# Kernel tuning notes

Hardware: AMD Instinct MI355X
Metric: run time of the kernel (lower is better)

The kernel has to match this reference:

```python
import jax, jax.numpy as jnp
import numpy as np

B = 64            # graphs per batch
NODES_PER_GRAPH = 1008  # 12 snapshots * 84 nodes
N = B * NODES_PER_GRAPH # 64512 total nodes
E = N * 16              # ~1M edges
SNAP = 12
SEG = 84
D_IN = 84
D_H = 128
EPS_BN = 1e-5


def setup_inputs() -> dict:
    key = jax.random.key(0)
    ks = jax.random.split(key, 20)
    s = 0.05  # small init scale for numerical sanity
    return {
        "x": jax.random.normal(ks[0], (N, D_IN), jnp.float32),
        "edge_index": jax.random.randint(ks[1], (2, E), 0, N, jnp.int64),
        "w1": jax.random.normal(ks[2], (D_IN, D_H), jnp.float32) * s,
        "b1": jax.random.normal(ks[3], (D_H,), jnp.float32) * s,
        "w2": jax.random.normal(ks[4], (D_H, D_H), jnp.float32) * s,
        "b2": jax.random.normal(ks[5], (D_H,), jnp.float32) * s,
        "pe": jax.random.normal(ks[6], (NODES_PER_GRAPH, D_H), jnp.float32) * s,
        "wf1": jax.random.normal(ks[7], (SNAP * 4 * D_H, 512), jnp.float32) * s,
        "bf1": jax.random.normal(ks[8], (512,), jnp.float32) * s,
        "g1": jnp.ones((512,), jnp.float32),
        "be1": jnp.zeros((512,), jnp.float32),
        "wf2": jax.random.normal(ks[9], (512, 32), jnp.float32) * s,
        "bf2": jax.random.normal(ks[10], (32,), jnp.float32) * s,
        "g2": jnp.ones((32,), jnp.float32),
        "be2": jnp.zeros((32,), jnp.float32),
        "wf3": jax.random.normal(ks[11], (32, 2), jnp.float32) * s,
        "bf3": jax.random.normal(ks[12], (2,), jnp.float32) * s,
    }


def _batch_norm(h, g, b):
    # training-mode BN: biased batch statistics, eps=1e-5 (torch default)
    mu = jnp.mean(h, axis=0)
    var = jnp.var(h, axis=0)
    return (h - mu) * jax.lax.rsqrt(var + EPS_BN) * g + b


def reference(x, edge_index, w1, b1, w2, b2, pe, wf1, bf1, g1, be1,
              wf2, bf2, g2, be2, wf3, bf3):
    src, dst = edge_index[0], edge_index[1]
    n = x.shape[0]
    b = n // NODES_PER_GRAPH

    # GINConv (eps=0, sum aggregation): h = Linear(x + sum_{j->i} x_j)
    agg1 = jax.ops.segment_sum(x[src], dst, num_segments=n)
    h1 = (x + agg1) @ w1 + b1                      # [N,128]
    agg2 = jax.ops.segment_sum(h1[src], dst, num_segments=n)
    h2 = (h1 + agg2) @ w2 + b2                     # [N,128]

    # positional encoding + full self-attention per graph (1008 tokens)
    h2 = h2.reshape(b, NODES_PER_GRAPH, D_H) + pe  # [B,1008,128]
    score = jnp.einsum('bqd,bkd->bqk', h2, h2) / np.sqrt(float(D_H))
    attn = jax.nn.softmax(score, axis=-1)
    ctx = jnp.einsum('bqk,bkd->bqd', attn, h2)     # [B,1008,128]

    # segmented max/mean pooling: blocks of 84 nodes, 12 snapshots per graph
    h1s = h1.reshape(b, SNAP, SEG, D_H)
    h2s = ctx.reshape(b, SNAP, SEG, D_H)
    feat = jnp.concatenate([
        jnp.max(h1s, axis=2), jnp.mean(h1s, axis=2),
        jnp.max(h2s, axis=2), jnp.mean(h2s, axis=2),
    ], axis=-1)                                    # [B,12,512]
    feat = feat.reshape(b, SNAP * 4 * D_H)         # [B,6144]

    # MLP head (dropout = identity at eval; BN in training-stat mode)
    out = _batch_norm(jax.nn.silu(feat @ wf1 + bf1), g1, be1)
    out = _batch_norm(jax.nn.silu(out @ wf2 + bf2), g2, be2)
    out = jax.nn.softmax(out @ wf3 + bf3, axis=1)  # [B,2]
    return out
```

## Files before the change

kernel.cpp:

```cpp
#include <hip/hip_runtime.h>
#include <math.h>

#define N_NODES 64512
#define DIN 84
#define XHP 96
#define KP 96
#define USP 104
#define DH 128
#define NPG 1008
#define BG 64
#define NSNAP 12
#define NSEG 84
#define NEDGE (N_NODES * 16)
#define DEGCAP 64
#define NBUCK 252
#define EPB 4096
#define BCAP 4608
#define ATT_SCALE 0.08838834764831845f

typedef __bf16 bf16_t;
typedef __bf16 bf16x8 __attribute__((ext_vector_type(8)));
typedef __bf16 bf16x4 __attribute__((ext_vector_type(4)));
typedef float f32x4 __attribute__((ext_vector_type(4)));
typedef _Float16 f16_t;
typedef _Float16 f16x4 __attribute__((ext_vector_type(4)));
typedef _Float16 f16x8 __attribute__((ext_vector_type(8)));

__device__ __forceinline__ f32x4 up4(f16x4 v) {
    return (f32x4){(float)v[0], (float)v[1], (float)v[2], (float)v[3]};
}

__global__ __launch_bounds__(256) void cvt_xh(const float* __restrict__ x,
                                              f16_t* __restrict__ xh,
                                              int* __restrict__ bucketTail) {
    int t = blockIdx.x * 256 + threadIdx.x;
    if (t < N_NODES * 21) {
        int node = t / 21;
        int c = t - node * 21;
        f32x4 v = *(const f32x4*)(x + (size_t)node * DIN + c * 4);
        f16x4 o;
        o[0] = (f16_t)v[0]; o[1] = (f16_t)v[1];
        o[2] = (f16_t)v[2]; o[3] = (f16_t)v[3];
        *(f16x4*)(xh + (size_t)node * XHP + c * 4) = o;
    }
    if (t * 4 < NBUCK) {
        int4 z = {0, 0, 0, 0};
        *(int4*)(bucketTail + t * 4) = z;
    }
}

__global__ __launch_bounds__(256) void epart(const int* __restrict__ src,
                                             const int* __restrict__ dst,
                                             int* __restrict__ bucketTail,
                                             unsigned int* __restrict__ rec) {
    __shared__ int lcnt[NBUCK];
    __shared__ int gbase[NBUCK];
    int tid = threadIdx.x;
    int e0 = blockIdx.x * EPB;
    for (int i = tid; i < NBUCK; i += 256) lcnt[i] = 0;
    __syncthreads();

    unsigned int r[16];
    unsigned short lp[16];
    unsigned short bk[16];
#pragma unroll
    for (int i = 0; i < 16; i++) {
        int e = e0 + tid + i * 256;
        int s = src[e], d = dst[e];
        r[i] = ((unsigned int)d << 16) | (unsigned int)s;
        int b = d >> 8;
        bk[i] = (unsigned short)b;
        lp[i] = (unsigned short)atomicAdd(&lcnt[b], 1);
    }
    __syncthreads();
    for (int i = tid; i < NBUCK; i += 256)
        gbase[i] = atomicAdd(&bucketTail[i], lcnt[i]);
    __syncthreads();
#pragma unroll
    for (int i = 0; i < 16; i++) {
        int b = bk[i];
        int g = gbase[b] + lp[i];
        if (g < BCAP) rec[(size_t)b * BCAP + g] = r[i];
    }
}

__global__ __launch_bounds__(256) void ebuild(const unsigned int* __restrict__ rec,
                                              const int* __restrict__ bucketTail,
                                              int* __restrict__ cnt,
                                              unsigned short* __restrict__ eidx) {
    __shared__ unsigned short stage[256 * 72];
    __shared__ int rb8[256 * 8];
    int tid = threadIdx.x;
    int b = blockIdx.x;
#pragma unroll
    for (int i = 0; i < 8; i++) rb8[tid + i * 256] = 0;
    __syncthreads();

    int n = min(bucketTail[b], BCAP);
    const unsigned int* rbp = rec + (size_t)b * BCAP;
    for (int i = tid; i < n; i += 256) {
        unsigned int rv = rbp[i];
        int ld = (rv >> 16) & 255;
        int rng = (rv & 0xffffu) >> 13;
        atomicAdd(&rb8[ld * 8 + rng], 1);
    }
    __syncthreads();
    {
        int s = 0;
#pragma unroll
        for (int r = 0; r < 8; r++) {
            int c = rb8[tid * 8 + r];
            rb8[tid * 8 + r] = s;
            s += c;
        }
        cnt[b * 256 + tid] = s;
    }
    __syncthreads();
    for (int i = tid; i < n; i += 256) {
        unsigned int rv = rbp[i];
        int ld = (rv >> 16) & 255;
        int rng = (rv & 0xffffu) >> 13;
        int p = atomicAdd(&rb8[ld * 8 + rng], 1);
        if (p < DEGCAP) stage[ld * 72 + p] = (unsigned short)(rv & 0xffffu);
    }
    __syncthreads();

    uint4* op = (uint4*)(eidx + (size_t)b * 256 * DEGCAP);
#pragma unroll
    for (int i = 0; i < 8; i++) {
        int ch = tid + i * 256;
        int node = ch >> 3, e0 = (ch & 7) << 3;
        op[ch] = *(const uint4*)&stage[node * 72 + e0];
    }
}

__global__ __launch_bounds__(128) void prep_w12(const float* __restrict__ w1,
                                                const float* __restrict__ w2,
                                                const float* __restrict__ b1,
                                                f16_t* __restrict__ w1hT,
                                                f16_t* __restrict__ w12hT,
                                                float* __restrict__ bvec) {
    __shared__ float rowv[DH];
    int r = blockIdx.x;
    int j = threadIdx.x;
    const float* srcv = (r < DIN) ? (w1 + (size_t)r * DH) : b1;
    rowv[j] = srcv[j];
    __syncthreads();
    float acc = 0.f;
#pragma unroll 4
    for (int k = 0; k < DH; k++) acc += rowv[k] * w2[k * DH + j];
    if (r < DIN) {
        w12hT[j * KP + r] = (f16_t)acc;
        w1hT[j * KP + r] = (f16_t)w1[(size_t)r * DH + j];
    } else {
        bvec[j] = acc;
        for (int k = DIN; k < KP; k++) {
            w1hT[j * KP + k] = (f16_t)0.f;
            w12hT[j * KP + k] = (f16_t)0.f;
        }
    }
}

__global__ __launch_bounds__(512) void gin1(const float* __restrict__ x,
                                            const f16_t* __restrict__ xh,
                                            const int* __restrict__ cnt,
                                            const unsigned short* __restrict__ eidx,
                                            const f16_t* __restrict__ w1hT,
                                            const float* __restrict__ b1,
                                            float* __restrict__ h1,
                                            f16_t* __restrict__ zh) {
    __shared__ f16_t us[32][USP];
    int n0 = blockIdx.x * 32;
    int tid = threadIdx.x;
    int grp = tid >> 4;
    int gl = tid & 15;
    int node = n0 + grp;
    int s = node * DEGCAP;
    int e = s + min(cnt[node], DEGCAP);
    bool has2 = gl < 5;

    const float* xn = x + (size_t)node * DIN;
    f32x4 a0 = *(const f32x4*)(xn + gl * 4);
    f32x4 a1 = has2 ? *(const f32x4*)(xn + 64 + gl * 4) : (f32x4){0.f, 0.f, 0.f, 0.f};

    int i = s;
    for (; i + 4 <= e; i += 4) {
        const f16_t* p0 = xh + (size_t)eidx[i] * XHP + gl * 4;
        const f16_t* p1 = xh + (size_t)eidx[i + 1] * XHP + gl * 4;
        const f16_t* p2 = xh + (size_t)eidx[i + 2] * XHP + gl * 4;
        const f16_t* p3 = xh + (size_t)eidx[i + 3] * XHP + gl * 4;
        a0 += up4(*(const f16x4*)p0) + up4(*(const f16x4*)p1) +
              up4(*(const f16x4*)p2) + up4(*(const f16x4*)p3);
        if (has2) {
            a1 += up4(*(const f16x4*)(p0 + 64)) + up4(*(const f16x4*)(p1 + 64)) +
                  up4(*(const f16x4*)(p2 + 64)) + up4(*(const f16x4*)(p3 + 64));
        }
    }
    for (; i < e; i++) {
        const f16_t* p0 = xh + (size_t)eidx[i] * XHP + gl * 4;
        a0 += up4(*(const f16x4*)p0);
        if (has2) a1 += up4(*(const f16x4*)(p0 + 64));
    }

    f16x4 z0;
    z0[0] = (f16_t)a0[0]; z0[1] = (f16_t)a0[1];
    z0[2] = (f16_t)a0[2]; z0[3] = (f16_t)a0[3];
    *(f16x4*)(zh + (size_t)node * XHP + gl * 4) = z0;
    *(f16x4*)&us[grp][gl * 4] = z0;
    if (has2) {
        f16x4 z1;
        z1[0] = (f16_t)a1[0]; z1[1] = (f16_t)a1[1];
        z1[2] = (f16_t)a1[2]; z1[3] = (f16_t)a1[3];
        *(f16x4*)(zh + (size_t)node * XHP + 64 + gl * 4) = z1;
        *(f16x4*)&us[grp][64 + gl * 4] = z1;
    }
    if (gl >= 5 && gl < 8) {
        f16x4 zz = {(f16_t)0.f, (f16_t)0.f, (f16_t)0.f, (f16_t)0.f};
        *(f16x4*)&us[grp][64 + gl * 4] = zz;
    }
    __syncthreads();

    int wv = tid >> 6, lane = tid & 63;
    int l15 = lane & 15, quad = lane >> 4;
    int dim = wv * 16 + l15;
    f32x4 acc[2];
    acc[0] = (f32x4){0.f, 0.f, 0.f, 0.f};
    acc[1] = (f32x4){0.f, 0.f, 0.f, 0.f};
#pragma unroll
    for (int ks = 0; ks < 3; ks++) {
        f16x8 bW = *(const f16x8*)(w1hT + (size_t)dim * KP + ks * 32 + quad * 8);
        f16x8 aU0 = *(const f16x8*)&us[l15][ks * 32 + quad * 8];
        f16x8 aU1 = *(const f16x8*)&us[16 + l15][ks * 32 + quad * 8];
        acc[0] = __builtin_amdgcn_mfma_f32_16x16x32_f16(aU0, bW, acc[0], 0, 0, 0);
        acc[1] = __builtin_amdgcn_mfma_f32_16x16x32_f16(aU1, bW, acc[1], 0, 0, 0);
    }
    float bias = b1[dim];
#pragma unroll
    for (int tm = 0; tm < 2; tm++) {
        int nb = n0 + tm * 16 + quad * 4;
#pragma unroll
        for (int r = 0; r < 4; r++)
            h1[(size_t)(nb + r) * DH + dim] = acc[tm][r] + bias;
    }
}

__global__ __launch_bounds__(512) void gin2(const f16_t* __restrict__ zh,
                                            const int* __restrict__ cnt,
                                            const unsigned short* __restrict__ eidx,
                                            const f16_t* __restrict__ w12hT,
                                            const float* __restrict__ bvec,
                                            const float* __restrict__ b2,
                                            const float* __restrict__ pe,
                                            bf16_t* __restrict__ h2bf,
                                            bf16_t* __restrict__ h2T) {
    __shared__ f16_t us[32][USP];
    __shared__ float sdeg[32];
    int n0 = blockIdx.x * 32;
    int tid = threadIdx.x;
    int grp = tid >> 4;
    int gl = tid & 15;
    int node = n0 + grp;
    int dg = min(cnt[node], DEGCAP);
    int s = node * DEGCAP;
    int e = s + dg;
    bool has2 = gl < 5;
    if (gl == 0) sdeg[grp] = (float)(1 + dg);

    const f16_t* zn = zh + (size_t)node * XHP;
    f32x4 a0 = up4(*(const f16x4*)(zn + gl * 4));
    f32x4 a1 = has2 ? up4(*(const f16x4*)(zn + 64 + gl * 4)) : (f32x4){0.f, 0.f, 0.f, 0.f};

    int i = s;
    for (; i + 4 <= e; i += 4) {
        const f16_t* p0 = zh + (size_t)eidx[i] * XHP + gl * 4;
        const f16_t* p1 = zh + (size_t)eidx[i + 1] * XHP + gl * 4;
        const f16_t* p2 = zh + (size_t)eidx[i + 2] * XHP + gl * 4;
        const f16_t* p3 = zh + (size_t)eidx[i + 3] * XHP + gl * 4;
        a0 += up4(*(const f16x4*)p0) + up4(*(const f16x4*)p1) +
              up4(*(const f16x4*)p2) + up4(*(const f16x4*)p3);
        if (has2) {
            a1 += up4(*(const f16x4*)(p0 + 64)) + up4(*(const f16x4*)(p1 + 64)) +
                  up4(*(const f16x4*)(p2 + 64)) + up4(*(const f16x4*)(p3 + 64));
        }
    }
    for (; i < e; i++) {
        const f16_t* p0 = zh + (size_t)eidx[i] * XHP + gl * 4;
        a0 += up4(*(const f16x4*)p0);
        if (has2) a1 += up4(*(const f16x4*)(p0 + 64));
    }
    f16x4 u0;
    u0[0] = (f16_t)a0[0]; u0[1] = (f16_t)a0[1];
    u0[2] = (f16_t)a0[2]; u0[3] = (f16_t)a0[3];
    *(f16x4*)&us[grp][gl * 4] = u0;
    if (has2) {
        f16x4 u1;
        u1[0] = (f16_t)a1[0]; u1[1] = (f16_t)a1[1];
        u1[2] = (f16_t)a1[2]; u1[3] = (f16_t)a1[3];
        *(f16x4*)&us[grp][64 + gl * 4] = u1;
    }
    if (gl >= 5 && gl < 8) {
        f16x4 zz = {(f16_t)0.f, (f16_t)0.f, (f16_t)0.f, (f16_t)0.f};
        *(f16x4*)&us[grp][64 + gl * 4] = zz;
    }
    __syncthreads();

    int wv = tid >> 6, lane = tid & 63;
    int l15 = lane & 15, quad = lane >> 4;
    int dim = wv * 16 + l15;
    f32x4 acc[2];
    acc[0] = (f32x4){0.f, 0.f, 0.f, 0.f};
    acc[1] = (f32x4){0.f, 0.f, 0.f, 0.f};
#pragma unroll
    for (int ks = 0; ks < 3; ks++) {
        f16x8 bW = *(const f16x8*)(w12hT + (size_t)dim * KP + ks * 32 + quad * 8);
        f16x8 aU0 = *(const f16x8*)&us[l15][ks * 32 + quad * 8];
        f16x8 aU1 = *(const f16x8*)&us[16 + l15][ks * 32 + quad * 8];
        acc[0] = __builtin_amdgcn_mfma_f32_16x16x32_f16(aU0, bW, acc[0], 0, 0, 0);
        acc[1] = __builtin_amdgcn_mfma_f32_16x16x32_f16(aU1, bW, acc[1], 0, 0, 0);
    }

    float bb = b2[dim];
    float bv = bvec[dim];
#pragma unroll
    for (int tm = 0; tm < 2; tm++) {
        int nb = n0 + tm * 16 + quad * 4;
        int bg = nb / NPG;
        int pos = nb - bg * NPG;
        bf16x4 tv;
#pragma unroll
        for (int r = 0; r < 4; r++) {
            float v = acc[tm][r] + bb + sdeg[tm * 16 + quad * 4 + r] * bv +
                      pe[(size_t)(pos + r) * DH + dim];
            bf16_t vb = (bf16_t)v;
            h2bf[(size_t)(nb + r) * DH + dim] = vb;
            tv[r] = vb;
        }
        *(bf16x4*)(h2T + ((size_t)bg * DH + dim) * NPG + pos) = tv;
    }
}

#define QTILE 128
#define KTILE 64
#define KS_PITCH 136
#define KT_PITCH 72
#define PS_PITCH 68
#define KT_OFF 8704

__global__ __launch_bounds__(256, 2) void attn_mfma(const bf16_t* __restrict__ h2bf,
                                                    const bf16_t* __restrict__ h2T,
                                                    float* __restrict__ ctx) {
    __shared__ __align__(16) bf16_t smem[KT_OFF + DH * KT_PITCH];

    int tid = threadIdx.x;
    int wv = tid >> 6, lane = tid & 63;
    int l15 = lane & 15, quad = lane >> 4;
    int idx = blockIdx.x;
    int xcd = idx & 7;
    int qt = (idx >> 3) & 7;
    int b = (idx >> 6) * 8 + xcd;
    const bf16_t* hb = h2bf + (size_t)b * NPG * DH;
    const bf16_t* hbT = h2T + (size_t)b * DH * NPG;

    bf16x8 bQ[2][4];
#pragma unroll
    for (int set = 0; set < 2; set++) {
        int qrow_frag = qt * QTILE + wv * 32 + set * 16 + l15;
        int qsrc = (qrow_frag < NPG) ? qrow_frag : 0;
#pragma unroll
        for (int kb = 0; kb < 4; kb++)
            bQ[set][kb] = *(const bf16x8*)(hb + (size_t)qsrc * DH + kb * 32 + quad * 8);
    }

    float m0 = -1e30f, li0 = 0.0f;
    float m1 = -1e30f, li1 = 0.0f;
    f32x4 O[2][8];
#pragma unroll
    for (int t = 0; t < 8; t++) {
        O[0][t] = (f32x4){0.f, 0.f, 0.f, 0.f};
        O[1][t] = (f32x4){0.f, 0.f, 0.f, 0.f};
    }

    uint4 rK[4], rT[4];
#define LOADR(KT_)                                                              \
    {                                                                           \
        int kt_ = (KT_);                                                        \
        _Pragma("unroll")                                                       \
        for (int i = 0; i < 4; i++) {                                           \
            int c = tid + i * 256;                                              \
            int row = c >> 4, seg = c & 15;                                     \
            int key = kt_ * KTILE + row;                                        \
            uint4 v = {0u, 0u, 0u, 0u};                                         \
            if (key < NPG) v = *(const uint4*)(hb + (size_t)key * DH + seg * 8);\
            rK[i] = v;                                                          \
        }                                                                       \
        _Pragma("unroll")                                                       \
        for (int i = 0; i < 4; i++) {                                           \
            int c = tid + i * 256;                                              \
            int dim = c >> 3, kc = c & 7;                                       \
            int key0 = kt_ * KTILE + kc * 8;                                    \
            uint4 v = {0u, 0u, 0u, 0u};                                         \
            if (key0 < NPG) v = *(const uint4*)(hbT + (size_t)dim * NPG + key0);\
            rT[i] = v;                                                          \
        }                                                                       \
    }

    LOADR(0);

    for (int kt = 0; kt < 16; kt++) {
        __syncthreads();
#pragma unroll
        for (int i = 0; i < 4; i++) {
            int c = tid + i * 256;
            int row = c >> 4, seg = c & 15;
            *(uint4*)&smem[row * KS_PITCH + seg * 8] = rK[i];
        }
#pragma unroll
        for (int i = 0; i < 4; i++) {
            int c = tid + i * 256;
            int dim = c >> 3, kc = c & 7;
            *(uint4*)&smem[KT_OFF + dim * KT_PITCH + kc * 8] = rT[i];
        }
        if (kt < 15) LOADR(kt + 1);
        __syncthreads();

        f32x4 S[2][4];
#pragma unroll
        for (int nt = 0; nt < 4; nt++) {
            S[0][nt] = (f32x4){0.f, 0.f, 0.f, 0.f};
            S[1][nt] = (f32x4){0.f, 0.f, 0.f, 0.f};
#pragma unroll
            for (int kb = 0; kb < 4; kb++) {
                bf16x8 aK = *(const bf16x8*)&smem[(nt * 16 + l15) * KS_PITCH + kb * 32 + quad * 8];
                S[0][nt] = __builtin_amdgcn_mfma_f32_16x16x32_bf16(aK, bQ[0][kb], S[0][nt], 0, 0, 0);
                S[1][nt] = __builtin_amdgcn_mfma_f32_16x16x32_bf16(aK, bQ[1][kb], S[1][nt], 0, 0, 0);
            }
        }
        __syncthreads();

        float pmax0 = -1e30f, pmax1 = -1e30f;
#pragma unroll
        for (int nt = 0; nt < 4; nt++) {
            bool valid = (kt * KTILE + nt * 16) < NPG;
#pragma unroll
            for (int r = 0; r < 4; r++) {
                float v0 = valid ? S[0][nt][r] * ATT_SCALE : -1e30f;
                float v1 = valid ? S[1][nt][r] * ATT_SCALE : -1e30f;
                S[0][nt][r] = v0;
                S[1][nt][r] = v1;
                pmax0 = fmaxf(pmax0, v0);
                pmax1 = fmaxf(pmax1, v1);
            }
        }
        pmax0 = fmaxf(pmax0, __shfl_xor(pmax0, 16));
        pmax0 = fmaxf(pmax0, __shfl_xor(pmax0, 32));
        pmax1 = fmaxf(pmax1, __shfl_xor(pmax1, 16));
        pmax1 = fmaxf(pmax1, __shfl_xor(pmax1, 32));
        float newm0 = fmaxf(m0, pmax0);
        float newm1 = fmaxf(m1, pmax1);

        float alpha0 = 1.0f, alpha1 = 1.0f;
        if (!__all((newm0 == m0) && (newm1 == m1))) {
            alpha0 = __expf(m0 - newm0);
            alpha1 = __expf(m1 - newm1);
            float a00 = __shfl(alpha0, quad * 4 + 0);
            float a01 = __shfl(alpha0, quad * 4 + 1);
            float a02 = __shfl(alpha0, quad * 4 + 2);
            float a03 = __shfl(alpha0, quad * 4 + 3);
            float a10 = __shfl(alpha1, quad * 4 + 0);
            float a11 = __shfl(alpha1, quad * 4 + 1);
            float a12 = __shfl(alpha1, quad * 4 + 2);
            float a13 = __shfl(alpha1, quad * 4 + 3);
#pragma unroll
            for (int t = 0; t < 8; t++) {
                O[0][t][0] *= a00; O[0][t][1] *= a01; O[0][t][2] *= a02; O[0][t][3] *= a03;
                O[1][t][0] *= a10; O[1][t][1] *= a11; O[1][t][2] *= a12; O[1][t][3] *= a13;
            }
        }
        m0 = newm0;
        m1 = newm1;

        float psum0 = 0.f, psum1 = 0.f;
#pragma unroll
        for (int nt = 0; nt < 4; nt++) {
            bf16x4 pk0, pk1;
#pragma unroll
            for (int r = 0; r < 4; r++) {
                float p0 = __expf(S[0][nt][r] - newm0);
                float p1 = __expf(S[1][nt][r] - newm1);
                psum0 += p0;
                psum1 += p1;
                pk0[r] = (bf16_t)p0;
                pk1[r] = (bf16_t)p1;
            }
            *(bf16x4*)&smem[(wv * 32 + l15) * PS_PITCH + nt * 16 + quad * 4] = pk0;
            *(bf16x4*)&smem[(wv * 32 + 16 + l15) * PS_PITCH + nt * 16 + quad * 4] = pk1;
        }
        psum0 += __shfl_xor(psum0, 16);
        psum0 += __shfl_xor(psum0, 32);
        psum1 += __shfl_xor(psum1, 16);
        psum1 += __shfl_xor(psum1, 32);
        li0 = li0 * alpha0 + psum0;
        li1 = li1 * alpha1 + psum1;

#pragma unroll
        for (int kb2 = 0; kb2 < 2; kb2++) {
            bf16x8 aP0 = *(const bf16x8*)&smem[(wv * 32 + l15) * PS_PITCH + kb2 * 32 + quad * 8];
            bf16x8 aP1 = *(const bf16x8*)&smem[(wv * 32 + 16 + l15) * PS_PITCH + kb2 * 32 + quad * 8];
#pragma unroll
            for (int t = 0; t < 8; t++) {
                bf16x8 bV = *(const bf16x8*)&smem[KT_OFF + (t * 16 + l15) * KT_PITCH + kb2 * 32 + quad * 8];
                O[0][t] = __builtin_amdgcn_mfma_f32_16x16x32_bf16(aP0, bV, O[0][t], 0, 0, 0);
                O[1][t] = __builtin_amdgcn_mfma_f32_16x16x32_bf16(aP1, bV, O[1][t], 0, 0, 0);
            }
        }
    }
#undef LOADR

    float invl0[4], invl1[4];
#pragma unroll
    for (int r = 0; r < 4; r++) {
        invl0[r] = 1.0f / __shfl(li0, quad * 4 + r);
        invl1[r] = 1.0f / __shfl(li1, quad * 4 + r);
    }
    float* cb = ctx + (size_t)b * NPG * DH;
#pragma unroll
    for (int t = 0; t < 8; t++)
#pragma unroll
        for (int r = 0; r < 4; r++) {
            int qrow0 = qt * QTILE + wv * 32 + quad * 4 + r;
            int qrow1 = qrow0 + 16;
            if (qrow0 < NPG) cb[(size_t)qrow0 * DH + t * 16 + l15] = O[0][t][r] * invl0[r];
            if (qrow1 < NPG) cb[(size_t)qrow1 * DH + t * 16 + l15] = O[1][t][r] * invl1[r];
        }
}

__global__ __launch_bounds__(128) void pooling(const float* __restrict__ h1,
                                               const float* __restrict__ ctx,
                                               const float* __restrict__ bf1,
                                               float* __restrict__ feat,
                                               float* __restrict__ y1raw) {
    int bs = blockIdx.x;
    int d = threadIdx.x;
    if (bs < 256) {
        int i = bs * 128 + d;
        y1raw[i] = bf1[i & 511];
    }
    int base = bs * NSEG;
    float mx1 = -1e30f, sm1 = 0.f, mx2 = -1e30f, sm2 = 0.f;
    for (int n = 0; n < NSEG; n++) {
        float v1 = h1[(size_t)(base + n) * DH + d];
        mx1 = fmaxf(mx1, v1);
        sm1 += v1;
        float v2 = ctx[(size_t)(base + n) * DH + d];
        mx2 = fmaxf(mx2, v2);
        sm2 += v2;
    }
    const float invs = 1.0f / NSEG;
    feat[bs * 512 + d] = mx1;
    feat[bs * 512 + 128 + d] = sm1 * invs;
    feat[bs * 512 + 256 + d] = mx2;
    feat[bs * 512 + 384 + d] = sm2 * invs;
}

#define MLP1_KCH 96
__global__ __launch_bounds__(256) void mlp1_splitk(const float* __restrict__ feat,
                                                   const float* __restrict__ wf1,
                                                   float* __restrict__ y1raw) {
    __shared__ float fl[64][MLP1_KCH];
    int k0 = blockIdx.y * MLP1_KCH;
    int tid = threadIdx.x;
    for (int c = tid; c < 64 * MLP1_KCH; c += 256) {
        int row = c / MLP1_KCH;
        int kk = c - row * MLP1_KCH;
        fl[row][kk] = feat[(size_t)row * 6144 + k0 + kk];
    }
    __syncthreads();
    int col = blockIdx.x * 128 + (tid & 127);
    int rbase = (tid >> 7) * 32;
    float acc[32];
#pragma unroll
    for (int r = 0; r < 32; r++) acc[r] = 0.f;
    for (int kg = 0; kg < MLP1_KCH; kg += 4) {
        float w0 = wf1[(size_t)(k0 + kg + 0) * 512 + col];
        float w1 = wf1[(size_t)(k0 + kg + 1) * 512 + col];
        float w2 = wf1[(size_t)(k0 + kg + 2) * 512 + col];
        float w3 = wf1[(size_t)(k0 + kg + 3) * 512 + col];
#pragma unroll
        for (int r = 0; r < 32; r++) {
            float4 f = *(const float4*)&fl[rbase + r][kg];
            acc[r] += f.x * w0 + f.y * w1 + f.z * w2 + f.w * w3;
        }
    }
#pragma unroll
    for (int r = 0; r < 32; r++)
        atomicAdd(&y1raw[(size_t)(rbase + r) * 512 + col], acc[r]);
}

__global__ __launch_bounds__(1024) void head_tail(const float* __restrict__ y1raw,
                                                  const float* __restrict__ g1,
                                                  const float* __restrict__ be1,
                                                  const float* __restrict__ wf2,
                                                  const float* __restrict__ bf2,
                                                  const float* __restrict__ g2,
                                                  const float* __restrict__ be2,
                                                  const float* __restrict__ wf3,
                                                  const float* __restrict__ bf3,
                                                  float* __restrict__ out) {
    __shared__ float sscale[512];
    __shared__ float sshift[512];
    __shared__ float zsm[64][68];
    __shared__ float y2sm[64][33];
    __shared__ float scale2[32], shift2[32];

    int tid = threadIdx.x;

    if (tid < 512) {
        float s = 0.f, s2 = 0.f;
        for (int b = 0; b < 64; b++) {
            float v = y1raw[b * 512 + tid];
            float h = v / (1.0f + __expf(-v));
            s += h;
            s2 += h * h;
        }
        float mu = s * (1.0f / 64.0f);
        float var = s2 * (1.0f / 64.0f) - mu * mu;
        float sc = rsqrtf(var + 1e-5f) * g1[tid];
        sscale[tid] = sc;
        sshift[tid] = be1[tid] - mu * sc;
    }
    __syncthreads();

    int b0 = tid >> 5;
    int b1 = b0 + 32;
    int j2 = tid & 31;
    float acc0 = bf2[j2], acc1 = acc0;
    for (int kc = 0; kc < 8; kc++) {
        __syncthreads();
#pragma unroll
        for (int c = 0; c < 4; c++) {
            int lin = tid + c * 1024;
            int bb = lin >> 6;
            int kk = lin & 63;
            int k = kc * 64 + kk;
            float v = y1raw[bb * 512 + k];
            float h = v / (1.0f + __expf(-v));
            zsm[bb][kk] = h * sscale[k] + sshift[k];
        }
        __syncthreads();
        for (int kk = 0; kk < 64; kk++) {
            float wv = wf2[(kc * 64 + kk) * 32 + j2];
            acc0 += zsm[b0][kk] * wv;
            acc1 += zsm[b1][kk] * wv;
        }
    }
    y2sm[b0][j2] = acc0;
    y2sm[b1][j2] = acc1;
    __syncthreads();

    if (tid < 32) {
        float s = 0.f, s2 = 0.f;
        for (int b = 0; b < 64; b++) {
            float h = y2sm[b][tid];
            float hs = h / (1.0f + __expf(-h));
            s += hs;
            s2 += hs * hs;
        }
        float mu = s * (1.0f / 64.0f);
        float var = s2 * (1.0f / 64.0f) - mu * mu;
        float sc = rsqrtf(var + 1e-5f) * g2[tid];
        scale2[tid] = sc;
        shift2[tid] = be2[tid] - mu * sc;
    }
    __syncthreads();

    if (tid < 64) {
        float l0 = bf3[0], l1 = bf3[1];
        for (int k = 0; k < 32; k++) {
            float h = y2sm[tid][k];
            float hs = h / (1.0f + __expf(-h));
            float v = hs * scale2[k] + shift2[k];
            l0 += v * wf3[k * 2 + 0];
            l1 += v * wf3[k * 2 + 1];
        }
        float m = fmaxf(l0, l1);
        float e0 = __expf(l0 - m), e1 = __expf(l1 - m);
        float inv = 1.0f / (e0 + e1);
        out[tid * 2 + 0] = e0 * inv;
        out[tid * 2 + 1] = e1 * inv;
    }
}

extern "C" void kernel_launch(void* const* d_in, const int* in_sizes, int n_in,
                              void* d_out, int out_size, void* d_ws, size_t ws_size,
                              hipStream_t stream) {
    const float* x   = (const float*)d_in[0];
    const int*   ei  = (const int*)d_in[1];
    const float* w1  = (const float*)d_in[2];
    const float* b1  = (const float*)d_in[3];
    const float* w2  = (const float*)d_in[4];
    const float* b2  = (const float*)d_in[5];
    const float* pe  = (const float*)d_in[6];
    const float* wf1 = (const float*)d_in[7];
    const float* bf1 = (const float*)d_in[8];
    const float* g1  = (const float*)d_in[9];
    const float* be1 = (const float*)d_in[10];
    const float* wf2 = (const float*)d_in[11];
    const float* bf2 = (const float*)d_in[12];
    const float* g2  = (const float*)d_in[13];
    const float* be2 = (const float*)d_in[14];
    const float* wf3 = (const float*)d_in[15];
    const float* bf3 = (const float*)d_in[16];
    float* out = (float*)d_out;

    const int* srcp = ei;
    const int* dstp = ei + NEDGE;

    float* ws = (float*)d_ws;
    size_t off = 0;
    float* h1   = ws + off; off += (size_t)N_NODES * DH;
    float* ctxb = ws + off; off += (size_t)N_NODES * DH;
    float* feat = ws + off; off += (size_t)BG * NSNAP * 512;
    bf16_t* h2bf = (bf16_t*)(ws + off); off += (size_t)N_NODES * DH / 2;
    bf16_t* h2T  = (bf16_t*)(ws + off); off += (size_t)N_NODES * DH / 2;
    f16_t* zh    = (f16_t*)(ws + off);  off += (size_t)N_NODES * XHP / 2;
    f16_t* xh    = (f16_t*)(ws + off);  off += (size_t)N_NODES * XHP / 2;
    float* y1raw = ws + off; off += 64 * 512;
    f16_t* w1hT  = (f16_t*)(ws + off);  off += (size_t)DH * KP / 2;
    f16_t* w12hT = (f16_t*)(ws + off);  off += (size_t)DH * KP / 2;
    float* bvec  = ws + off; off += DH;
    int* bucketTail = (int*)(ws + off); off += NBUCK;
    int* cnt  = (int*)(ws + off); off += N_NODES;
    unsigned int* rec = (unsigned int*)(ws + off); off += (size_t)NBUCK * BCAP;
    unsigned short* eidx = (unsigned short*)(ws + off);

    cvt_xh<<<(N_NODES * 21 + 255) / 256, 256, 0, stream>>>(x, xh, bucketTail);
    prep_w12<<<DIN + 1, 128, 0, stream>>>(w1, w2, b1, w1hT, w12hT, bvec);
    epart<<<NEDGE / EPB, 256, 0, stream>>>(srcp, dstp, bucketTail, rec);
    ebuild<<<NBUCK, 256, 0, stream>>>(rec, bucketTail, cnt, eidx);

    gin1<<<N_NODES / 32, 512, 0, stream>>>(x, xh, cnt, eidx, w1hT, b1, h1, zh);
    gin2<<<N_NODES / 32, 512, 0, stream>>>(zh, cnt, eidx, w12hT, bvec, b2, pe, h2bf, h2T);
    attn_mfma<<<BG * 8, 256, 0, stream>>>(h2bf, h2T, ctxb);
    pooling<<<BG * NSNAP, 128, 0, stream>>>(h1, ctxb, bf1, feat, y1raw);
    mlp1_splitk<<<dim3(4, 64), 256, 0, stream>>>(feat, wf1, y1raw);
    head_tail<<<1, 1024, 0, stream>>>(y1raw, g1, be1, wf2, bf2, g2, be2, wf3, bf3, out);
}
```

Measured before the change: 364.2 us.

## Use single-wave attention blocks that read K/V directly from global memory

```diff
diff --git a/kernel.cpp b/kernel.cpp
--- a/kernel.cpp
+++ b/kernel.cpp
@@ -339,32 +339,27 @@
     }
 }
 
-#define QTILE 128
 #define KTILE 64
-#define KS_PITCH 136
-#define KT_PITCH 72
-#define PS_PITCH 68
-#define KT_OFF 8704
-
-__global__ __launch_bounds__(256, 2) void attn_mfma(const bf16_t* __restrict__ h2bf,
-                                                    const bf16_t* __restrict__ h2T,
-                                                    float* __restrict__ ctx) {
-    __shared__ __align__(16) bf16_t smem[KT_OFF + DH * KT_PITCH];
-
-    int tid = threadIdx.x;
-    int wv = tid >> 6, lane = tid & 63;
+#define PS_PITCH 72
+
+__global__ __launch_bounds__(64) void attn_mfma(const bf16_t* __restrict__ h2bf,
+                                                const bf16_t* __restrict__ h2T,
+                                                float* __restrict__ ctx) {
+    __shared__ __align__(16) bf16_t ps[32 * PS_PITCH];
+
+    int lane = threadIdx.x;
     int l15 = lane & 15, quad = lane >> 4;
     int idx = blockIdx.x;
     int xcd = idx & 7;
-    int qt = (idx >> 3) & 7;
-    int b = (idx >> 6) * 8 + xcd;
+    int chunk = (idx >> 3) & 31;
+    int b = (idx >> 8) * 8 + xcd;
     const bf16_t* hb = h2bf + (size_t)b * NPG * DH;
     const bf16_t* hbT = h2T + (size_t)b * DH * NPG;
 
     bf16x8 bQ[2][4];
 #pragma unroll
     for (int set = 0; set < 2; set++) {
-        int qrow_frag = qt * QTILE + wv * 32 + set * 16 + l15;
+        int qrow_frag = chunk * 32 + set * 16 + l15;
         int qsrc = (qrow_frag < NPG) ? qrow_frag : 0;
 #pragma unroll
         for (int kb = 0; kb < 4; kb++)
@@ -379,63 +374,25 @@
         O[0][t] = (f32x4){0.f, 0.f, 0.f, 0.f};
         O[1][t] = (f32x4){0.f, 0.f, 0.f, 0.f};
     }
-
-    uint4 rK[4], rT[4];
-#define LOADR(KT_)                                                              \
-    {                                                                           \
-        int kt_ = (KT_);                                                        \
-        _Pragma("unroll")                                                       \
-        for (int i = 0; i < 4; i++) {                                           \
-            int c = tid + i * 256;                                              \
-            int row = c >> 4, seg = c & 15;                                     \
-            int key = kt_ * KTILE + row;                                        \
-            uint4 v = {0u, 0u, 0u, 0u};                                         \
-            if (key < NPG) v = *(const uint4*)(hb + (size_t)key * DH + seg * 8);\
-            rK[i] = v;                                                          \
-        }                                                                       \
-        _Pragma("unroll")                                                       \
-        for (int i = 0; i < 4; i++) {                                           \
-            int c = tid + i * 256;                                              \
-            int dim = c >> 3, kc = c & 7;                                       \
-            int key0 = kt_ * KTILE + kc * 8;                                    \
-            uint4 v = {0u, 0u, 0u, 0u};                                         \
-            if (key0 < NPG) v = *(const uint4*)(hbT + (size_t)dim * NPG + key0);\
-            rT[i] = v;                                                          \
-        }                                                                       \
-    }
-
-    LOADR(0);
+    const bf16x8 zerov = {(bf16_t)0.f, (bf16_t)0.f, (bf16_t)0.f, (bf16_t)0.f,
+                          (bf16_t)0.f, (bf16_t)0.f, (bf16_t)0.f, (bf16_t)0.f};
 
     for (int kt = 0; kt < 16; kt++) {
-        __syncthreads();
-#pragma unroll
-        for (int i = 0; i < 4; i++) {
-            int c = tid + i * 256;
-            int row = c >> 4, seg = c & 15;
-            *(uint4*)&smem[row * KS_PITCH + seg * 8] = rK[i];
-        }
-#pragma unroll
-        for (int i = 0; i < 4; i++) {
-            int c = tid + i * 256;
-            int dim = c >> 3, kc = c & 7;
-            *(uint4*)&smem[KT_OFF + dim * KT_PITCH + kc * 8] = rT[i];
-        }
-        if (kt < 15) LOADR(kt + 1);
-        __syncthreads();
-
         f32x4 S[2][4];
 #pragma unroll
         for (int nt = 0; nt < 4; nt++) {
+            bool valid = (kt * KTILE + nt * 16) < NPG;
             S[0][nt] = (f32x4){0.f, 0.f, 0.f, 0.f};
             S[1][nt] = (f32x4){0.f, 0.f, 0.f, 0.f};
 #pragma unroll
             for (int kb = 0; kb < 4; kb++) {
-                bf16x8 aK = *(const bf16x8*)&smem[(nt * 16 + l15) * KS_PITCH + kb * 32 + quad * 8];
+                bf16x8 aK = valid
+                    ? *(const bf16x8*)(hb + (size_t)(kt * KTILE + nt * 16 + l15) * DH + kb * 32 + quad * 8)
+                    : zerov;
                 S[0][nt] = __builtin_amdgcn_mfma_f32_16x16x32_bf16(aK, bQ[0][kb], S[0][nt], 0, 0, 0);
                 S[1][nt] = __builtin_amdgcn_mfma_f32_16x16x32_bf16(aK, bQ[1][kb], S[1][nt], 0, 0, 0);
             }
         }
-        __syncthreads();
 
         float pmax0 = -1e30f, pmax1 = -1e30f;
 #pragma unroll
@@ -492,8 +449,8 @@
                 pk0[r] = (bf16_t)p0;
                 pk1[r] = (bf16_t)p1;
             }
-            *(bf16x4*)&smem[(wv * 32 + l15) * PS_PITCH + nt * 16 + quad * 4] = pk0;
-            *(bf16x4*)&smem[(wv * 32 + 16 + l15) * PS_PITCH + nt * 16 + quad * 4] = pk1;
+            *(bf16x4*)&ps[l15 * PS_PITCH + nt * 16 + quad * 4] = pk0;
+            *(bf16x4*)&ps[(16 + l15) * PS_PITCH + nt * 16 + quad * 4] = pk1;
         }
         psum0 += __shfl_xor(psum0, 16);
         psum0 += __shfl_xor(psum0, 32);
@@ -504,17 +461,20 @@
 
 #pragma unroll
         for (int kb2 = 0; kb2 < 2; kb2++) {
-            bf16x8 aP0 = *(const bf16x8*)&smem[(wv * 32 + l15) * PS_PITCH + kb2 * 32 + quad * 8];
-            bf16x8 aP1 = *(const bf16x8*)&smem[(wv * 32 + 16 + l15) * PS_PITCH + kb2 * 32 + quad * 8];
+            bf16x8 aP0 = *(const bf16x8*)&ps[l15 * PS_PITCH + kb2 * 32 + quad * 8];
+            bf16x8 aP1 = *(const bf16x8*)&ps[(16 + l15) * PS_PITCH + kb2 * 32 + quad * 8];
+            int key0 = kt * KTILE + kb2 * 32 + quad * 8;
+            bool kvalid = key0 < NPG;
 #pragma unroll
             for (int t = 0; t < 8; t++) {
-                bf16x8 bV = *(const bf16x8*)&smem[KT_OFF + (t * 16 + l15) * KT_PITCH + kb2 * 32 + quad * 8];
+                bf16x8 bV = kvalid
+                    ? *(const bf16x8*)(hbT + (size_t)(t * 16 + l15) * NPG + key0)
+                    : zerov;
                 O[0][t] = __builtin_amdgcn_mfma_f32_16x16x32_bf16(aP0, bV, O[0][t], 0, 0, 0);
                 O[1][t] = __builtin_amdgcn_mfma_f32_16x16x32_bf16(aP1, bV, O[1][t], 0, 0, 0);
             }
         }
     }
-#undef LOADR
 
     float invl0[4], invl1[4];
 #pragma unroll
@@ -527,7 +487,7 @@
     for (int t = 0; t < 8; t++)
 #pragma unroll
         for (int r = 0; r < 4; r++) {
-            int qrow0 = qt * QTILE + wv * 32 + quad * 4 + r;
+            int qrow0 = chunk * 32 + quad * 4 + r;
             int qrow1 = qrow0 + 16;
             if (qrow0 < NPG) cb[(size_t)qrow0 * DH + t * 16 + l15] = O[0][t][r] * invl0[r];
             if (qrow1 < NPG) cb[(size_t)qrow1 * DH + t * 16 + l15] = O[1][t][r] * invl1[r];
@@ -740,7 +700,7 @@
 
     gin1<<<N_NODES / 32, 512, 0, stream>>>(x, xh, cnt, eidx, w1hT, b1, h1, zh);
     gin2<<<N_NODES / 32, 512, 0, stream>>>(zh, cnt, eidx, w12hT, bvec, b2, pe, h2bf, h2T);
-    attn_mfma<<<BG * 8, 256, 0, stream>>>(h2bf, h2T, ctxb);
+    attn_mfma<<<BG * 32, 64, 0, stream>>>(h2bf, h2T, ctxb);
     pooling<<<BG * NSNAP, 128, 0, stream>>>(h1, ctxb, bf1, feat, y1raw);
     mlp1_splitk<<<dim3(4, 64), 256, 0, stream>>>(feat, wf1, y1raw);
     head_tail<<<1, 1024, 0, stream>>>(y1raw, g1, be1, wf2, bf2, g2, be2, wf3, bf3, out);
```

Result: slower. 543.0 us (+49.1%).
